# Kernel optimization log

Measured on AMD Instinct MI355X. Metric: run time of the kernel, lower is better.

The kernel has to match this reference:

```python
import jax, jax.numpy as jnp
import numpy as np

B, T, NIN, N, NOUT = 64, 512, 64, 1024, 32
DT, TAU = 1.0, 10.0
STATE_STD, RATE_STD, OUT_STD = 0.05, 0.05, 0.05
HIDDEN_G = 1.0


def retanh(x):
    return jnp.maximum(jnp.tanh(x), 0.0)


def setup_inputs() -> dict:
    key = jax.random.key(0)
    ks = jax.random.split(key, 10)
    u = jax.random.normal(ks[0], (B, T, NIN), jnp.float32)
    x_0 = jnp.zeros((N,), jnp.float32)
    state_noise = STATE_STD * jax.random.normal(ks[1], (B, T, N), jnp.float32)
    rate_noise = RATE_STD * jax.random.normal(ks[2], (B, T, N), jnp.float32)
    output_noise = OUT_STD * jax.random.normal(ks[3], (B, T, NOUT), jnp.float32)
    W_in = jax.random.normal(ks[4], (N, NIN), jnp.float32) / np.sqrt(NIN).astype(np.float32)
    b_in = 0.1 + 0.01 * jax.random.normal(ks[5], (N,), jnp.float32)
    W_rec = jax.random.normal(ks[6], (N, N), jnp.float32) * (HIDDEN_G / np.sqrt(N).astype(np.float32))
    W_rec = W_rec * (1.0 - jnp.eye(N, dtype=jnp.float32))  # zero self-connections
    lim = 1.0 / np.sqrt(N).astype(np.float32)
    W_out = jax.random.uniform(ks[7], (NOUT, N), jnp.float32, -lim, lim)
    b_out = jax.random.uniform(ks[8], (NOUT,), jnp.float32, -lim, lim)
    return {"u": u, "x_0": x_0, "state_noise": state_noise, "rate_noise": rate_noise,
            "output_noise": output_noise, "W_in": W_in, "b_in": b_in, "W_rec": W_rec,
            "W_out": W_out, "b_out": b_out}


def reference(u, x_0, state_noise, rate_noise, output_noise, W_in, b_in, W_rec, W_out, b_out):
    alpha = DT / TAU
    # time-major for scan: [T, B, ...]
    u_t = jnp.swapaxes(u, 0, 1)
    sn = jnp.swapaxes(state_noise, 0, 1)
    rn = jnp.swapaxes(rate_noise, 0, 1)
    on = jnp.swapaxes(output_noise, 0, 1)
    x0 = jnp.broadcast_to(x_0, (B, N))
    r0 = retanh(x0)

    def step(carry, inp):
        x, r = carry
        ut, snt, rnt, ont = inp
        x_next = x + alpha * (-x + r @ W_rec.T + ut @ W_in.T + b_in + snt)
        r_next = retanh(x_next) + rnt
        z_next = r_next @ W_out.T + b_out + ont
        return (x_next, r_next), (x_next, r_next, z_next)

    _, (X, R, Z) = jax.lax.scan(step, (x0, r0), (u_t, sn, rn, on))
    # back to batch-major [B, T, ...]
    return (jnp.swapaxes(X, 0, 1), jnp.swapaxes(R, 0, 1), jnp.swapaxes(Z, 0, 1))
```

## Files before the change

kernel.cpp:

```cpp
#include <hip/hip_runtime.h>
#include <hip/hip_bf16.h>
#include <stdint.h>

#define B_    64
#define T_    512
#define NIN_  64
#define N_    1024
#define NOUT_ 32

#define NISL  16
#define BPI   16
#define MB    4
#define COLS  64
#define NT    4
#define KW    256
#define KT    8

typedef float f32x4 __attribute__((ext_vector_type(4)));
typedef short s16x8 __attribute__((ext_vector_type(8)));

__device__ __forceinline__ unsigned short f2bf(float f) {
  union { float f; unsigned u; } v; v.f = f;
  unsigned r = v.u + 0x7FFFu + ((v.u >> 16) & 1u);
  return (unsigned short)(r >> 16);
}

__device__ __forceinline__ s16x8 ld_ex16(const unsigned* p) {
  s16x8 r;
  asm volatile("global_load_dwordx4 %0, %1, off sc1"
               : "=v"(r) : "v"(p) : "memory");
  return r;
}

__global__ __launch_bounds__(256, 1) void rnn_scan(
    const float* __restrict__ U, const float* __restrict__ X0,
    const float* __restrict__ SN, const float* __restrict__ RN,
    const float* __restrict__ Wi, const float* __restrict__ Bi,
    const float* __restrict__ Wr,
    float* __restrict__ X, float* __restrict__ R,
    unsigned* __restrict__ flags, unsigned* __restrict__ ex)
{
  const int bid   = blockIdx.x;
  const int isl   = bid / BPI, slice = bid % BPI;
  const int tid   = threadIdx.x;
  const int wave  = tid >> 6, lane = tid & 63;
  const int l15   = lane & 15, koct = lane >> 4;
  const int colbase = slice * COLS;

  s16x8 bfrag[KT][NT];
#pragma unroll
  for (int kt = 0; kt < KT; ++kt) {
    const int k0 = wave * KW + kt * 32 + koct * 8;
#pragma unroll
    for (int nt = 0; nt < NT; ++nt) {
      const float* p = Wr + (size_t)(colbase + nt * 16 + l15) * N_ + k0;
      s16x8 f;
#pragma unroll
      for (int i = 0; i < 8; ++i) f[i] = (short)f2bf(p[i]);
      bfrag[kt][nt] = f;
    }
  }
  s16x8 wifrag[NT];
  if (wave < 2) {
#pragma unroll
    for (int nt = 0; nt < NT; ++nt) {
      const float* p = Wi + (size_t)(colbase + nt * 16 + l15) * NIN_ + wave * 32 + koct * 8;
      s16x8 f;
#pragma unroll
      for (int i = 0; i < 8; ++i) f[i] = (short)f2bf(p[i]);
      wifrag[nt] = f;
    }
  }

  const int cc  = lane;
  const int bloc = wave;
  const int bg  = isl * MB + bloc;
  const int nn  = colbase + cc;
  const int abatch = isl * MB + (l15 & (MB - 1));

  float x = X0[nn];
  const float bin = Bi[nn];
  const float r0 = fmaxf(tanhf(x), 0.f);

  __shared__ float part[4][COLS][MB];

  unsigned* const myflags = flags + isl * (T_ + 1);

  {
    unsigned short h = f2bf(r0);
    unsigned other = __shfl_xor((unsigned)h, 1);
    if ((lane & 1) == 0)
      __hip_atomic_store(ex + (size_t)bg * (N_ / 2) + (nn >> 1),
                         (unsigned)h | (other << 16),
                         __ATOMIC_RELAXED, __HIP_MEMORY_SCOPE_AGENT);
  }
  __syncthreads();
  if (tid == 0)
    __hip_atomic_fetch_add(myflags, 1u, __ATOMIC_RELAXED, __HIP_MEMORY_SCOPE_AGENT);

  float pxn = 0.f, prv = 0.f;

  for (int t = 0; t < T_; ++t) {
    const int par = t & 1;
    const size_t row = (size_t)bg * T_ + t;

    const float snv = SN[row * N_ + nn];
    const float rnv = RN[row * N_ + nn];
    s16x8 ua;
    if (wave < 2) {
      const float* p = U + ((size_t)(isl * MB + (l15 & (MB - 1))) * T_ + t) * NIN_
                         + wave * 32 + koct * 8;
#pragma unroll
      for (int i = 0; i < 8; ++i) ua[i] = (short)f2bf(p[i]);
    }

    while (__hip_atomic_load(myflags + t, __ATOMIC_RELAXED, __HIP_MEMORY_SCOPE_AGENT) < BPI)
      __builtin_amdgcn_s_sleep(2);

    if (t > 0) {
      X[(row - 1) * N_ + nn] = pxn;
      R[(row - 1) * N_ + nn] = prv;
    }

    const unsigned* exr = ex + (size_t)par * (B_ * (N_ / 2))
                             + (size_t)abatch * (N_ / 2);
    s16x8 afr[KT];
#pragma unroll
    for (int kt = 0; kt < KT; ++kt)
      afr[kt] = ld_ex16(exr + ((wave * KW + kt * 32 + koct * 8) >> 1));
    asm volatile("s_waitcnt vmcnt(0)" ::: "memory");
    __builtin_amdgcn_sched_barrier(0);

    f32x4 acc[NT];
#pragma unroll
    for (int nt = 0; nt < NT; ++nt) acc[nt] = f32x4{0.f, 0.f, 0.f, 0.f};
#pragma unroll
    for (int kt = 0; kt < KT; ++kt)
#pragma unroll
      for (int nt = 0; nt < NT; ++nt)
        acc[nt] = __builtin_amdgcn_mfma_f32_16x16x32_bf16(afr[kt], bfrag[kt][nt], acc[nt], 0, 0, 0);
    if (wave < 2) {
#pragma unroll
      for (int nt = 0; nt < NT; ++nt)
        acc[nt] = __builtin_amdgcn_mfma_f32_16x16x32_bf16(ua, wifrag[nt], acc[nt], 0, 0, 0);
    }

    if (lane < 16) {
#pragma unroll
      for (int nt = 0; nt < NT; ++nt)
        *(f32x4*)&part[wave][nt * 16 + lane][0] = acc[nt];
    }
    __syncthreads();
    const float mat = part[0][cc][bloc] + part[1][cc][bloc] +
                      part[2][cc][bloc] + part[3][cc][bloc];
    const float xn = x + 0.1f * (-x + mat + bin + snv);
    const float rv = fmaxf(tanhf(xn), 0.f) + rnv;
    x = xn;

    {
      unsigned short h = f2bf(rv);
      unsigned other = __shfl_xor((unsigned)h, 1);
      if ((lane & 1) == 0)
        __hip_atomic_store(ex + (size_t)(par ^ 1) * (B_ * (N_ / 2)) +
                               (size_t)bg * (N_ / 2) + (nn >> 1),
                           (unsigned)h | (other << 16),
                           __ATOMIC_RELAXED, __HIP_MEMORY_SCOPE_AGENT);
    }
    __syncthreads();
    if (tid == 0)
      __hip_atomic_fetch_add(myflags + t + 1, 1u, __ATOMIC_RELAXED, __HIP_MEMORY_SCOPE_AGENT);

    pxn = xn; prv = rv;
  }
  {
    const size_t lrow = (size_t)bg * T_ + (T_ - 1);
    X[lrow * N_ + nn] = pxn;
    R[lrow * N_ + nn] = prv;
  }
}

#define TCH 128
__global__ __launch_bounds__(256, 1) void rnn_zout(
    const float* __restrict__ Rm, const float* __restrict__ ON,
    const float* __restrict__ Wo, const float* __restrict__ Bo,
    float* __restrict__ Z)
{
  const int bid = blockIdx.x;
  const int b = bid >> 2, tq = bid & 3;
  const int tid = threadIdx.x;
  const int o = tid & 31, kc = tid >> 5;

  float4 wv[32];
  const float4* wp = (const float4*)(Wo + (size_t)o * N_ + kc * 128);
#pragma unroll
  for (int i = 0; i < 32; ++i) wv[i] = wp[i];

  __shared__ float Rl[N_];
  __shared__ float zred[8][32];

  for (int t = tq * TCH; t < tq * TCH + TCH; ++t) {
    const size_t row = (size_t)b * T_ + t;
    ((float4*)Rl)[tid] = ((const float4*)(Rm + row * N_))[tid];
    __syncthreads();
    float a0 = 0.f;
#pragma unroll
    for (int i = 0; i < 32; ++i) {
      const float* rp = Rl + kc * 128 + i * 4;
      a0 += wv[i].x * rp[0] + wv[i].y * rp[1] + wv[i].z * rp[2] + wv[i].w * rp[3];
    }
    zred[kc][o] = a0;
    __syncthreads();
    if (tid < 32) {
      float z = Bo[tid];
#pragma unroll
      for (int k = 0; k < 8; ++k) z += zred[k][tid];
      Z[row * NOUT_ + tid] = z + ON[row * NOUT_ + tid];
    }
  }
}

extern "C" void kernel_launch(void* const* d_in, const int* in_sizes, int n_in,
                              void* d_out, int out_size, void* d_ws, size_t ws_size,
                              hipStream_t stream) {
  const float* U  = (const float*)d_in[0];
  const float* X0 = (const float*)d_in[1];
  const float* SN = (const float*)d_in[2];
  const float* RN = (const float*)d_in[3];
  const float* ON = (const float*)d_in[4];
  const float* Wi = (const float*)d_in[5];
  const float* Bi = (const float*)d_in[6];
  const float* Wr = (const float*)d_in[7];
  const float* Wo = (const float*)d_in[8];
  const float* Bo = (const float*)d_in[9];

  float* X = (float*)d_out;
  float* R = X + (size_t)B_ * T_ * N_;
  float* Z = R + (size_t)B_ * T_ * N_;

  unsigned* flags = (unsigned*)d_ws;
  unsigned* ex    = (unsigned*)((char*)d_ws + 65536);

  hipMemsetAsync(flags, 0, NISL * (T_ + 1) * sizeof(unsigned), stream);

  hipLaunchKernelGGL(rnn_scan, dim3(NISL * BPI), dim3(256), 0, stream,
                     U, X0, SN, RN, Wi, Bi, Wr, X, R, flags, ex);
  hipLaunchKernelGGL(rnn_zout, dim3(B_ * (T_ / TCH)), dim3(256), 0, stream,
                     R, ON, Wo, Bo, Z);
}
```

Before: 1.583 ms.

## Vectorize loads, swizzle LDS partials, and double-buffer z-output kernel

The scan kernel now loads W_rec, W_in and u as float4 pairs instead of scalar loads. It replaces the inline-asm sc1 load plus full vmcnt wait with per-dword relaxed atomic loads, and defers the bf16 conversion of u until after the MFMA loop. LDS partial-sum writes are XOR-swizzled to reduce bank conflicts. The z-output kernel halves its time chunk to double the block count, allows 2 blocks per CU, and double-buffers the R row load with one barrier per step. The four dword atomic loads may issue more memory instructions than one dwordx4 on the latency-critical exchange path.

After: 1.629 ms. 2.9% more time.

```diff
diff --git a/kernel.cpp b/kernel.cpp
--- a/kernel.cpp
+++ b/kernel.cpp
@@ -25,11 +25,19 @@
   return (unsigned short)(r >> 16);
 }
 
-__device__ __forceinline__ s16x8 ld_ex16(const unsigned* p) {
-  s16x8 r;
-  asm volatile("global_load_dwordx4 %0, %1, off sc1"
-               : "=v"(r) : "v"(p) : "memory");
-  return r;
+__device__ __forceinline__ s16x8 cvt8(float4 a, float4 b) {
+  s16x8 f;
+  f[0] = (short)f2bf(a.x); f[1] = (short)f2bf(a.y);
+  f[2] = (short)f2bf(a.z); f[3] = (short)f2bf(a.w);
+  f[4] = (short)f2bf(b.x); f[5] = (short)f2bf(b.y);
+  f[6] = (short)f2bf(b.z); f[7] = (short)f2bf(b.w);
+  return f;
+}
+
+__device__ __forceinline__ s16x8 pack4(unsigned a, unsigned b, unsigned c, unsigned d) {
+  union { unsigned u[4]; s16x8 v; } x;
+  x.u[0] = a; x.u[1] = b; x.u[2] = c; x.u[3] = d;
+  return x.v;
 }
 
 __global__ __launch_bounds__(256, 1) void rnn_scan(
@@ -53,30 +61,24 @@
     const int k0 = wave * KW + kt * 32 + koct * 8;
 #pragma unroll
     for (int nt = 0; nt < NT; ++nt) {
-      const float* p = Wr + (size_t)(colbase + nt * 16 + l15) * N_ + k0;
-      s16x8 f;
-#pragma unroll
-      for (int i = 0; i < 8; ++i) f[i] = (short)f2bf(p[i]);
-      bfrag[kt][nt] = f;
+      const float4* q = (const float4*)(Wr + (size_t)(colbase + nt * 16 + l15) * N_ + k0);
+      bfrag[kt][nt] = cvt8(q[0], q[1]);
     }
   }
   s16x8 wifrag[NT];
   if (wave < 2) {
 #pragma unroll
     for (int nt = 0; nt < NT; ++nt) {
-      const float* p = Wi + (size_t)(colbase + nt * 16 + l15) * NIN_ + wave * 32 + koct * 8;
-      s16x8 f;
-#pragma unroll
-      for (int i = 0; i < 8; ++i) f[i] = (short)f2bf(p[i]);
-      wifrag[nt] = f;
-    }
-  }
-
-  const int cc  = lane;
+      const float4* q = (const float4*)(Wi + (size_t)(colbase + nt * 16 + l15) * NIN_ + wave * 32 + koct * 8);
+      wifrag[nt] = cvt8(q[0], q[1]);
+    }
+  }
+
+  const int cc   = lane;
   const int bloc = wave;
-  const int bg  = isl * MB + bloc;
-  const int nn  = colbase + cc;
-  const int abatch = isl * MB + (l15 & (MB - 1));
+  const int bg   = isl * MB + bloc;
+  const int nn   = colbase + cc;
+  const int abatch = isl * MB + (l15 & 3);
 
   float x = X0[nn];
   const float bin = Bi[nn];
@@ -106,12 +108,11 @@
 
     const float snv = SN[row * N_ + nn];
     const float rnv = RN[row * N_ + nn];
-    s16x8 ua;
+    float4 uq0, uq1;
     if (wave < 2) {
-      const float* p = U + ((size_t)(isl * MB + (l15 & (MB - 1))) * T_ + t) * NIN_
-                         + wave * 32 + koct * 8;
-#pragma unroll
-      for (int i = 0; i < 8; ++i) ua[i] = (short)f2bf(p[i]);
+      const float4* q = (const float4*)(U + ((size_t)(isl * MB + (l15 & 3)) * T_ + t) * NIN_
+                                          + wave * 32 + koct * 8);
+      uq0 = q[0]; uq1 = q[1];
     }
 
     while (__hip_atomic_load(myflags + t, __ATOMIC_RELAXED, __HIP_MEMORY_SCOPE_AGENT) < BPI)
@@ -126,10 +127,14 @@
                              + (size_t)abatch * (N_ / 2);
     s16x8 afr[KT];
 #pragma unroll
-    for (int kt = 0; kt < KT; ++kt)
-      afr[kt] = ld_ex16(exr + ((wave * KW + kt * 32 + koct * 8) >> 1));
-    asm volatile("s_waitcnt vmcnt(0)" ::: "memory");
-    __builtin_amdgcn_sched_barrier(0);
+    for (int kt = 0; kt < KT; ++kt) {
+      const unsigned* p = exr + ((wave * KW + kt * 32 + koct * 8) >> 1);
+      unsigned q0 = __hip_atomic_load(p + 0, __ATOMIC_RELAXED, __HIP_MEMORY_SCOPE_AGENT);
+      unsigned q1 = __hip_atomic_load(p + 1, __ATOMIC_RELAXED, __HIP_MEMORY_SCOPE_AGENT);
+      unsigned q2 = __hip_atomic_load(p + 2, __ATOMIC_RELAXED, __HIP_MEMORY_SCOPE_AGENT);
+      unsigned q3 = __hip_atomic_load(p + 3, __ATOMIC_RELAXED, __HIP_MEMORY_SCOPE_AGENT);
+      afr[kt] = pack4(q0, q1, q2, q3);
+    }
 
     f32x4 acc[NT];
 #pragma unroll
@@ -140,6 +145,7 @@
       for (int nt = 0; nt < NT; ++nt)
         acc[nt] = __builtin_amdgcn_mfma_f32_16x16x32_bf16(afr[kt], bfrag[kt][nt], acc[nt], 0, 0, 0);
     if (wave < 2) {
+      s16x8 ua = cvt8(uq0, uq1);
 #pragma unroll
       for (int nt = 0; nt < NT; ++nt)
         acc[nt] = __builtin_amdgcn_mfma_f32_16x16x32_bf16(ua, wifrag[nt], acc[nt], 0, 0, 0);
@@ -147,12 +153,18 @@
 
     if (lane < 16) {
 #pragma unroll
-      for (int nt = 0; nt < NT; ++nt)
-        *(f32x4*)&part[wave][nt * 16 + lane][0] = acc[nt];
+      for (int nt = 0; nt < NT; ++nt) {
+        const int s = (nt * 2 + (lane >> 3)) & 3;
+        f32x4 a = acc[nt];
+        if (s & 1) a = f32x4{a[1], a[0], a[3], a[2]};
+        if (s & 2) a = f32x4{a[2], a[3], a[0], a[1]};
+        *(f32x4*)&part[wave][nt * 16 + lane][0] = a;
+      }
     }
     __syncthreads();
-    const float mat = part[0][cc][bloc] + part[1][cc][bloc] +
-                      part[2][cc][bloc] + part[3][cc][bloc];
+    const int sr = (cc >> 3) & 3;
+    const float mat = part[0][cc][bloc ^ sr] + part[1][cc][bloc ^ sr] +
+                      part[2][cc][bloc ^ sr] + part[3][cc][bloc ^ sr];
     const float xn = x + 0.1f * (-x + mat + bin + snv);
     const float rv = fmaxf(tanhf(xn), 0.f) + rnv;
     x = xn;
@@ -179,14 +191,14 @@
   }
 }
 
-#define TCH 128
-__global__ __launch_bounds__(256, 1) void rnn_zout(
+#define TCH 64
+__global__ __launch_bounds__(256, 2) void rnn_zout(
     const float* __restrict__ Rm, const float* __restrict__ ON,
     const float* __restrict__ Wo, const float* __restrict__ Bo,
     float* __restrict__ Z)
 {
   const int bid = blockIdx.x;
-  const int b = bid >> 2, tq = bid & 3;
+  const int b = bid >> 3, tq = bid & 7;
   const int tid = threadIdx.x;
   const int o = tid & 31, kc = tid >> 5;
 
@@ -194,26 +206,35 @@
   const float4* wp = (const float4*)(Wo + (size_t)o * N_ + kc * 128);
 #pragma unroll
   for (int i = 0; i < 32; ++i) wv[i] = wp[i];
-
-  __shared__ float Rl[N_];
-  __shared__ float zred[8][32];
-
-  for (int t = tq * TCH; t < tq * TCH + TCH; ++t) {
-    const size_t row = (size_t)b * T_ + t;
-    ((float4*)Rl)[tid] = ((const float4*)(Rm + row * N_))[tid];
-    __syncthreads();
+  const float bo = Bo[o];
+
+  __shared__ float Rl[2][N_];
+  __shared__ float zred[2][8][32];
+
+  const int t0 = tq * TCH;
+  ((float4*)Rl[0])[tid] = ((const float4*)(Rm + ((size_t)b * T_ + t0) * N_))[tid];
+  __syncthreads();
+
+  for (int i = 0; i < TCH; ++i) {
+    const int cur = i & 1;
+    const size_t row = (size_t)b * T_ + t0 + i;
+    float4 nx;
+    if (i + 1 < TCH)
+      nx = ((const float4*)(Rm + (row + 1) * N_))[tid];
     float a0 = 0.f;
 #pragma unroll
-    for (int i = 0; i < 32; ++i) {
-      const float* rp = Rl + kc * 128 + i * 4;
-      a0 += wv[i].x * rp[0] + wv[i].y * rp[1] + wv[i].z * rp[2] + wv[i].w * rp[3];
-    }
-    zred[kc][o] = a0;
+    for (int j = 0; j < 32; ++j) {
+      const float* rp = &Rl[cur][kc * 128 + j * 4];
+      a0 += wv[j].x * rp[0] + wv[j].y * rp[1] + wv[j].z * rp[2] + wv[j].w * rp[3];
+    }
+    if (i + 1 < TCH)
+      ((float4*)Rl[cur ^ 1])[tid] = nx;
+    zred[cur][kc][o] = a0;
     __syncthreads();
     if (tid < 32) {
-      float z = Bo[tid];
-#pragma unroll
-      for (int k = 0; k < 8; ++k) z += zred[k][tid];
+      float z = bo;
+#pragma unroll
+      for (int k = 0; k < 8; ++k) z += zred[cur][k][tid];
       Z[row * NOUT_ + tid] = z + ON[row * NOUT_ + tid];
     }
   }
```
